# Kernel optimization log

Measured on AMD Instinct MI355X. Metric: run time of the kernel, lower is better.

The kernel has to match this reference:

```python
import jax, jax.numpy as jnp
import numpy as np

N_EMBD = 2048
N_HEAD = 8          # config.n_head // 2
HEAD_DIM = 256      # n_embd // (n_head // 2)
HALF = HEAD_DIM // 2
LAMBDA_INIT = 0.8
RMS_EPS = 1.1920929e-07  # torch float32 finfo eps (F.rms_norm default)


def _rms_norm(x):
    # F.rms_norm with no weight: x / sqrt(mean(x^2) + eps)
    return x * jax.lax.rsqrt(jnp.mean(x * x, axis=-1, keepdims=True) + RMS_EPS)


def setup_inputs() -> dict:
    key = jax.random.key(0)
    ks = jax.random.split(key, 10)
    B, T, C = 2, 2048, N_EMBD
    x = jax.random.normal(ks[0], (B, T, C), dtype=jnp.float32)
    wq = jax.random.normal(ks[1], (C, C), dtype=jnp.float32) * 0.02
    wk = jax.random.normal(ks[2], (C, C), dtype=jnp.float32) * 0.02
    wv = jax.random.normal(ks[3], (C, C), dtype=jnp.float32) * 0.02
    wo = jax.random.normal(ks[4], (C, C), dtype=jnp.float32) * 0.02
    lq1 = jax.random.normal(ks[5], (HEAD_DIM,), dtype=jnp.float32) * 0.1
    lk1 = jax.random.normal(ks[6], (HEAD_DIM,), dtype=jnp.float32) * 0.1
    lq2 = jax.random.normal(ks[7], (HEAD_DIM,), dtype=jnp.float32) * 0.1
    lk2 = jax.random.normal(ks[8], (HEAD_DIM,), dtype=jnp.float32) * 0.1
    return {"x": x, "wq": wq, "wk": wk, "wv": wv, "wo": wo,
            "lq1": lq1, "lk1": lk1, "lq2": lq2, "lk2": lk2}


def _causal_attn(q, k, v, mask):
    # q,k: [B,H,T,half], v: [B,H,T,HEAD_DIM]
    scale = 1.0 / jnp.sqrt(jnp.asarray(q.shape[-1], q.dtype))
    scores = jnp.einsum('bhqd,bhkd->bhqk', q, k) * scale
    scores = jnp.where(mask, scores, -jnp.inf)
    attn = jax.nn.softmax(scores, axis=-1)
    return jnp.einsum('bhqk,bhkd->bhqd', attn, v)


def reference(x, wq, wk, wv, wo, lq1, lk1, lq2, lk2):
    B, T, C = x.shape
    lambda_1 = jnp.exp(jnp.sum(lq1 * lk1))
    lambda_2 = jnp.exp(jnp.sum(lq2 * lk2))
    lambda_full = lambda_1 - lambda_2 + LAMBDA_INIT

    q = (x @ wq.T).reshape(B, T, N_HEAD, 2, HALF).transpose(0, 2, 1, 3, 4)  # [B,H,T,2,half]
    k = (x @ wk.T).reshape(B, T, N_HEAD, 2, HALF).transpose(0, 2, 1, 3, 4)
    v = (x @ wv.T).reshape(B, T, N_HEAD, HEAD_DIM).transpose(0, 2, 1, 3)    # [B,H,T,hd]

    q1 = _rms_norm(q[..., 0, :]); q2 = _rms_norm(q[..., 1, :])
    k1 = _rms_norm(k[..., 0, :]); k2 = _rms_norm(k[..., 1, :])

    mask = jnp.tril(jnp.ones((T, T), dtype=bool))
    y1 = _causal_attn(q1, k1, v, mask)
    y2 = _causal_attn(q2, k2, v, mask)
    y = y1 - lambda_full * y2                                               # [B,H,T,hd]

    y = y.transpose(0, 2, 1, 3).reshape(B, T, C)
    return (y @ wo.T) * (1.0 - LAMBDA_INIT)
```

## Files before the change

kernel.cpp:

```cpp
#include <hip/hip_runtime.h>
#include <stdint.h>


typedef __bf16 bf16;
typedef bf16 bf16x8 __attribute__((ext_vector_type(8)));
typedef bf16 bf16x4 __attribute__((ext_vector_type(4)));
typedef float f32x4 __attribute__((ext_vector_type(4)));

typedef void __attribute__((address_space(1)))* gas_t;
typedef void __attribute__((address_space(3)))* las_t;

__device__ __forceinline__ void gload16(const void* g, void* l) {
  __builtin_amdgcn_global_load_lds((gas_t)(uintptr_t)g, (las_t)(uint32_t)(uintptr_t)l, 16, 0, 0);
}

__device__ __forceinline__ f32x4 mfma16x16(bf16x8 a, bf16x8 b, f32x4 c) {
  return __builtin_amdgcn_mfma_f32_16x16x32_bf16(a, b, c, 0, 0, 0);
}

__global__ __launch_bounds__(256) void cast_all(const float* __restrict__ x,
                                                const float* __restrict__ wq, const float* __restrict__ wk,
                                                const float* __restrict__ wv, const float* __restrict__ wo,
                                                const float* __restrict__ lq1, const float* __restrict__ lk1,
                                                const float* __restrict__ lq2, const float* __restrict__ lk2,
                                                bf16* __restrict__ xb,
                                                bf16* __restrict__ wqb, bf16* __restrict__ wkb,
                                                bf16* __restrict__ wvb, bf16* __restrict__ wob,
                                                float* __restrict__ lam) {
  __shared__ float red[8];
  int tid = threadIdx.x;
  int i = blockIdx.x * 256 + tid;
  const float* in;
  bf16* out;
  int j;
  if (i < 2097152) {
    in = x; out = xb; j = i;
  } else {
    int k = i - 2097152;
    int w = k >> 20;
    j = k & 1048575;
    in = (w == 0) ? wq : (w == 1) ? wk : (w == 2) ? wv : wo;
    out = (w == 0) ? wqb : (w == 1) ? wkb : (w == 2) ? wvb : wob;
  }
  float4 v = ((const float4*)in)[j];
  bf16x4 o;
  o[0] = (bf16)v.x; o[1] = (bf16)v.y; o[2] = (bf16)v.z; o[3] = (bf16)v.w;
  ((bf16x4*)out)[j] = o;

  if (blockIdx.x == 0) {
    float a = lq1[tid] * lk1[tid];
    float b = lq2[tid] * lk2[tid];
#pragma unroll
    for (int m = 32; m >= 1; m >>= 1) {
      a += __shfl_xor(a, m, 64);
      b += __shfl_xor(b, m, 64);
    }
    if ((tid & 63) == 0) { red[tid >> 6] = a; red[4 + (tid >> 6)] = b; }
    __syncthreads();
    if (tid == 0) {
      float s1 = red[0] + red[1] + red[2] + red[3];
      float s2 = red[4] + red[5] + red[6] + red[7];
      lam[0] = expf(s1) - expf(s2) + 0.8f;
    }
  }
}

__global__ __launch_bounds__(512, 2) void gemm_qkv8(const bf16* __restrict__ A,
                                                    const bf16* __restrict__ Bq,
                                                    const bf16* __restrict__ Bk,
                                                    const bf16* __restrict__ Bv,
                                                    bf16* __restrict__ Cq, bf16* __restrict__ Ck,
                                                    bf16* __restrict__ Cv) {
  __shared__ char lds[98304];
  const int K = 2048, nt = 64;

  int p = blockIdx.y * gridDim.x + blockIdx.x;
  int lid = (p & 7) * 48 + (p >> 3);
  const int bm = (lid / 24) * 256;
  const int bnG = (lid % 24) * 256;
  const int z = bnG >> 11;
  const int bn = bnG & 2047;
  const bf16* B = (z == 0) ? Bq : ((z == 1) ? Bk : Bv);

  const int tid = threadIdx.x;
  const int wid = tid >> 6, lane = tid & 63;
  const int l15 = lane & 15, lhi = lane >> 4;
  const int wm = wid >> 2, wn = wid & 3;

  const bf16* aS0 = A + (size_t)(bm + wid * 16 + l15) * K + lhi * 8;
  const bf16* bS0 = B + (size_t)(bn + wid * 16 + l15) * K + lhi * 8;

  auto stA = [&](int t, int pb) {
    char* d = lds + pb * 32768 + wid * 1024;
    const bf16* s = aS0 + t * 32;
    gload16(s, d);
    gload16(s + (size_t)128 * K, d + 8192);
  };
  auto stB = [&](int t, int pb) {
    char* d = lds + pb * 32768 + 16384 + wid * 1024;
    const bf16* s = bS0 + t * 32;
    gload16(s, d);
    gload16(s + (size_t)128 * K, d + 8192);
  };

  const f32x4 fz = {0.f, 0.f, 0.f, 0.f};
  f32x4 acc[8][4];
#pragma unroll
  for (int m = 0; m < 8; ++m)
#pragma unroll
    for (int n = 0; n < 4; ++n) acc[m][n] = fz;

  stA(0, 0); stB(0, 0);
  stA(1, 1); stB(1, 1);
  asm volatile("s_waitcnt vmcnt(4)" ::: "memory");
  __builtin_amdgcn_s_barrier();

  int cur = 0;
  for (int t = 0; t < nt; ++t) {
    const char* ab = lds + cur * 32768;
    const char* bb = ab + 16384;
    int nx2 = cur + 2; if (nx2 >= 3) nx2 -= 3;
    bf16x8 a[8], b0, b1;

#pragma unroll
    for (int m = 0; m < 8; ++m) a[m] = *(const bf16x8*)(ab + (wm * 8 + m) * 1024 + lane * 16);
    b0 = *(const bf16x8*)(bb + (wn * 4 + 0) * 1024 + lane * 16);
    b1 = *(const bf16x8*)(bb + (wn * 4 + 1) * 1024 + lane * 16);
    if (t + 2 < nt) stA(t + 2, nx2);
    __builtin_amdgcn_s_barrier();
    __builtin_amdgcn_s_setprio(1);
#pragma unroll
    for (int m = 0; m < 8; ++m) {
      acc[m][0] = mfma16x16(a[m], b0, acc[m][0]);
      acc[m][1] = mfma16x16(a[m], b1, acc[m][1]);
    }
    __builtin_amdgcn_s_setprio(0);
    __builtin_amdgcn_s_barrier();

    b0 = *(const bf16x8*)(bb + (wn * 4 + 2) * 1024 + lane * 16);
    b1 = *(const bf16x8*)(bb + (wn * 4 + 3) * 1024 + lane * 16);
    if (t + 2 < nt) stB(t + 2, nx2);
    __builtin_amdgcn_s_barrier();
    __builtin_amdgcn_s_setprio(1);
#pragma unroll
    for (int m = 0; m < 8; ++m) {
      acc[m][2] = mfma16x16(a[m], b0, acc[m][2]);
      acc[m][3] = mfma16x16(a[m], b1, acc[m][3]);
    }
    __builtin_amdgcn_s_setprio(0);
    if (t + 2 < nt) {
      asm volatile("s_waitcnt vmcnt(4)" ::: "memory");
    } else {
      asm volatile("s_waitcnt vmcnt(0)" ::: "memory");
    }
    __builtin_amdgcn_s_barrier();

    cur = (cur == 2) ? 0 : cur + 1;
  }

  if (z == 2) {
#pragma unroll
    for (int m = 0; m < 8; ++m)
#pragma unroll
      for (int n = 0; n < 4; ++n)
#pragma unroll
        for (int r = 0; r < 4; ++r) {
          int row = bm + wm * 128 + m * 16 + lhi * 4 + r;
          int col = bn + wn * 64 + n * 16 + l15;
          int bb3 = row >> 11, tt = row & 2047;
          Cv[(size_t)bb3 * 2048 * 2048 + (size_t)col * 2048 + tt] = (bf16)acc[m][n][r];
        }
    return;
  }
  float* ldsf = (float*)lds;
#pragma unroll
  for (int m = 0; m < 8; ++m)
#pragma unroll
    for (int r = 0; r < 4; ++r) {
      float s = acc[m][0][r] * acc[m][0][r] + acc[m][1][r] * acc[m][1][r] +
                acc[m][2][r] * acc[m][2][r] + acc[m][3][r] * acc[m][3][r];
      s += __shfl_xor(s, 1, 64);
      s += __shfl_xor(s, 2, 64);
      s += __shfl_xor(s, 4, 64);
      s += __shfl_xor(s, 8, 64);
      if (l15 == 0) ldsf[(wm * 128 + m * 16 + lhi * 4 + r) * 4 + wn] = s;
    }
  __syncthreads();
  const float osc = (z == 0) ? 0.08838834764831845f : 1.0f;
  bf16* C = (z == 0) ? Cq : Ck;
#pragma unroll
  for (int m = 0; m < 8; ++m) {
#pragma unroll
    for (int r = 0; r < 4; ++r) {
      int rl = wm * 128 + m * 16 + lhi * 4 + r;
      float tot = ldsf[rl * 4 + (wn & 2)] + ldsf[rl * 4 + (wn & 2) + 1];
      float sc = rsqrtf(tot * (1.0f / 128.0f) + 1.1920929e-07f) * osc;
#pragma unroll
      for (int n = 0; n < 4; ++n) {
        int col = bn + wn * 64 + n * 16 + l15;
        C[(size_t)(bm + rl) * 2048 + col] = (bf16)(acc[m][n][r] * sc);
      }
    }
  }
}

__global__ __launch_bounds__(512) void gemm_out(const bf16* __restrict__ A, const bf16* __restrict__ B,
                                                float* __restrict__ Cf) {
  __shared__ char lds[73728];
  const int K = 2048, nt = 64;

  int p = blockIdx.x;
  int lid = (p & 7) * 32 + (p >> 3);
  const int bm = (lid >> 4) * 256;
  const int bn = (lid & 15) * 128;

  const int tid = threadIdx.x;
  const int wid = tid >> 6, lane = tid & 63;
  const int l15 = lane & 15, lhi = lane >> 4;
  const int wm = wid >> 1, wn = wid & 1;

  const bf16* aB = A + (size_t)(bm + wid * 16 + l15) * K + lhi * 8;
  const bf16* bB = B + (size_t)(bn + wid * 16 + l15) * K + lhi * 8;

  auto stage = [&](int t, int pb) {
    char* base = lds + pb * 24576;
    const int k0 = t * 32;
    gload16(aB + k0, base + wid * 1024);
    gload16(aB + (size_t)128 * K + k0, base + 8192 + wid * 1024);
    gload16(bB + k0, base + 16384 + wid * 1024);
  };

  const f32x4 fz = {0.f, 0.f, 0.f, 0.f};
  f32x4 acc[4][4];
#pragma unroll
  for (int m = 0; m < 4; ++m)
#pragma unroll
    for (int n = 0; n < 4; ++n) acc[m][n] = fz;

  stage(0, 0);
  stage(1, 1);
  asm volatile("s_waitcnt vmcnt(3)" ::: "memory");
  __builtin_amdgcn_s_barrier();

  for (int t = 0; t < nt; ++t) {
    const char* ab = lds + (t % 3) * 24576;
    if (t + 2 < nt) stage(t + 2, (t + 2) % 3);
    bf16x8 a[4], b[4];
#pragma unroll
    for (int m = 0; m < 4; ++m)
      a[m] = *(const bf16x8*)(ab + (wm * 4 + m) * 1024 + lane * 16);
#pragma unroll
    for (int n = 0; n < 4; ++n)
      b[n] = *(const bf16x8*)(ab + 16384 + (wn * 4 + n) * 1024 + lane * 16);
    __builtin_amdgcn_s_setprio(1);
#pragma unroll
    for (int m = 0; m < 4; ++m)
#pragma unroll
      for (int n = 0; n < 4; ++n) acc[m][n] = mfma16x16(a[m], b[n], acc[m][n]);
    __builtin_amdgcn_s_setprio(0);
    if (t + 2 < nt) {
      asm volatile("s_waitcnt vmcnt(3)" ::: "memory");
    } else {
      asm volatile("s_waitcnt vmcnt(0)" ::: "memory");
    }
    __builtin_amdgcn_s_barrier();
  }

#pragma unroll
  for (int m = 0; m < 4; ++m)
#pragma unroll
    for (int n = 0; n < 4; ++n)
#pragma unroll
      for (int r = 0; r < 4; ++r) {
        int row = bm + wm * 64 + m * 16 + lhi * 4 + r;
        int col = bn + wn * 64 + n * 16 + l15;
        Cf[(size_t)row * 2048 + col] = acc[m][n][r] * 0.2f;
      }
}

__global__ __launch_bounds__(512, 4) void attn_kernel(const bf16* __restrict__ qb, const bf16* __restrict__ kb,
                                                      const bf16* __restrict__ vtb, bf16* __restrict__ yb,
                                                      const float* __restrict__ lamp) {
  __shared__ char lds[73728];
  const int tid = threadIdx.x;
  const int wid = tid >> 6, lane = tid & 63;
  const int l15 = lane & 15, lhi = lane >> 4;
  char* pl = lds + 65536 + wid * 1024;
  const int s = wid >> 2;
  const int rg = wid & 3;

  const int p = blockIdx.x;
  const int bh = p & 15;
  const int qt = (p < 256) ? (31 - (p >> 4)) : ((p - 256) >> 4);
  const int b = bh >> 3, h = bh & 7;
  const int wr0 = qt * 64 + rg * 16;
  const float lam = lamp[0];

  bf16x8 qf[4];
  {
    const bf16* qrow = qb + (size_t)(b * 2048 + wr0 + l15) * 2048 + h * 256 + s * 128 + lhi * 8;
#pragma unroll
    for (int c = 0; c < 4; ++c) qf[c] = *(const bf16x8*)(qrow + c * 32);
  }

  const f32x4 fz = {0.f, 0.f, 0.f, 0.f};
  f32x4 y[16];
#pragma unroll
  for (int f = 0; f < 16; ++f) y[f] = fz;
  float lsum[4] = {0.f, 0.f, 0.f, 0.f};

  const int nkt = 2 * qt + 2;
  const bf16* kbase = kb + (size_t)(b * 2048) * 2048 + h * 256;
  const bf16* vbase = vtb + (size_t)b * 2048 * 2048 + (size_t)(h * 256) * 2048;

  auto stage = [&](int kt2, int pp) {
    const int t0 = kt2 * 32;
#pragma unroll
    for (int c = 0; c < 2; ++c) {
      int cc = wid * 2 + c;
      int ss = cc >> 3, tg = (cc >> 2) & 1, kc = cc & 3;
      const bf16* sp = kbase + (size_t)(t0 + tg * 16 + l15) * 2048 + ss * 128 + kc * 32 + lhi * 8;
      gload16(sp, lds + pp * 16384 + ss * 8192 + tg * 4096 + kc * 1024);
    }
#pragma unroll
    for (int c = 0; c < 2; ++c) {
      int cc = wid * 2 + c;
      int i = cc >> 2, w4 = cc & 3;
      const bf16* vp = vbase + (size_t)(i * 64 + w4 * 16 + l15) * 2048 + t0 + lhi * 8;
      gload16(vp, lds + 32768 + pp * 16384 + cc * 1024);
    }
  };

  stage(0, 0);
  __syncthreads();

  for (int kt = 0; kt < nkt; ++kt) {
    const int cur = kt & 1;
    const int t0 = kt * 32;
    const bool active = (t0 <= wr0 + 15);
    if (kt + 1 < nkt) stage(kt + 1, cur ^ 1);
    if (active) {
      const char* kc = lds + cur * 16384 + s * 8192;
      const char* vc = lds + 32768 + cur * 16384;
      f32x4 sg[2];
      __builtin_amdgcn_s_setprio(1);
#pragma unroll
      for (int g = 0; g < 2; ++g) {
        f32x4 a = fz;
#pragma unroll
        for (int ks = 0; ks < 4; ++ks)
          a = mfma16x16(qf[ks], *(const bf16x8*)(kc + (g * 4096 + ks * 1024) + lane * 16), a);
        sg[g] = a;
      }
      __builtin_amdgcn_s_setprio(0);
      if (t0 + 31 > wr0) {
#pragma unroll
        for (int g = 0; g < 2; ++g) {
          int col = t0 + g * 16 + l15;
#pragma unroll
          for (int r = 0; r < 4; ++r) {
            int row = wr0 + lhi * 4 + r;
            if (col > row) sg[g][r] = -1e30f;
          }
        }
      }
#pragma unroll
      for (int g = 0; g < 2; ++g)
#pragma unroll
        for (int r = 0; r < 4; ++r) {
          float pv = __expf(sg[g][r] - 12.0f);
          lsum[r] += pv;
          *(bf16*)(pl + ((lhi * 4 + r) * 32 + g * 16 + l15) * 2) = (bf16)pv;
        }
      bf16x8 pa = *(const bf16x8*)(pl + (l15 * 32 + lhi * 8) * 2);
      __builtin_amdgcn_s_setprio(1);
#pragma unroll
      for (int f = 0; f < 16; ++f) {
        bf16x8 vf = *(const bf16x8*)(vc + (f * 64 + lane) * 16);
        y[f] = mfma16x16(pa, vf, y[f]);
      }
      __builtin_amdgcn_s_setprio(0);
    }
    __syncthreads();
  }

  float inv[4];
#pragma unroll
  for (int r = 0; r < 4; ++r) {
    float sv = lsum[r];
    sv += __shfl_xor(sv, 1, 64);
    sv += __shfl_xor(sv, 2, 64);
    sv += __shfl_xor(sv, 4, 64);
    sv += __shfl_xor(sv, 8, 64);
    inv[r] = (s == 0) ? (1.f / sv) : (lam / sv);
  }
  __syncthreads();
  float* yx = (float*)lds;
  if (s == 0) {
#pragma unroll
    for (int f = 0; f < 16; ++f)
#pragma unroll
      for (int r = 0; r < 4; ++r) {
        int rl = rg * 16 + lhi * 4 + r;
        yx[rl * 256 + f * 16 + l15] = y[f][r] * inv[r];
      }
  }
  __syncthreads();
  if (s == 1) {
#pragma unroll
    for (int r = 0; r < 4; ++r) {
      int rl = rg * 16 + lhi * 4 + r;
      bf16* orow = yb + (size_t)(b * 2048 + qt * 64 + rl) * 2048 + h * 256 + l15;
#pragma unroll
      for (int f = 0; f < 16; ++f) {
        float v = yx[rl * 256 + f * 16 + l15] - y[f][r] * inv[r];
        orow[f * 16] = (bf16)v;
      }
    }
  }
}

extern "C" void kernel_launch(void* const* d_in, const int* in_sizes, int n_in,
                              void* d_out, int out_size, void* d_ws, size_t ws_size,
                              hipStream_t stream) {
  const float* x = (const float*)d_in[0];
  const float* wq = (const float*)d_in[1];
  const float* wk = (const float*)d_in[2];
  const float* wv = (const float*)d_in[3];
  const float* wo = (const float*)d_in[4];
  const float* lq1 = (const float*)d_in[5];
  const float* lk1 = (const float*)d_in[6];
  const float* lq2 = (const float*)d_in[7];
  const float* lk2 = (const float*)d_in[8];
  float* out = (float*)d_out;
  char* ws = (char*)d_ws;

  if (ws_size < 117440516) return;

  bf16* xb = (bf16*)(ws + 0);
  bf16* wqb = (bf16*)(ws + 16777216);
  bf16* wkb = (bf16*)(ws + 25165824);
  bf16* wvb = (bf16*)(ws + 33554432);
  bf16* wob = (bf16*)(ws + 41943040);
  bf16* qbuf = (bf16*)(ws + 50331648);
  bf16* kbuf = (bf16*)(ws + 67108864);
  bf16* vtb = (bf16*)(ws + 83886080);
  bf16* ybuf = (bf16*)(ws + 100663296);
  float* lam = (float*)(ws + 117440512);

  cast_all<<<24576, 256, 0, stream>>>(x, wq, wk, wv, wo, lq1, lk1, lq2, lk2,
                                      xb, wqb, wkb, wvb, wob, lam);

  gemm_qkv8<<<dim3(24, 16), 512, 0, stream>>>(xb, wqb, wkb, wvb, qbuf, kbuf, vtb);

  attn_kernel<<<512, 512, 0, stream>>>(qbuf, kbuf, vtb, ybuf, lam);

  gemm_out<<<256, 512, 0, stream>>>(ybuf, wob, out);
}
```

Baseline: 301.5 us.

## Shrink QKV GEMM tile to 256x128 with a simpler single-stage pipeline

Retiles the fused QKV projection GEMM from 256x256 to 256x128 output tiles. This doubles the grid to 768 one-dimensional blocks with an XCD-aware block-to-tile mapping, and raises the launch-bounds occupancy hint. The main loop now stages A and B together and runs one 4x4 MFMA block per k-step with a single barrier, instead of the split half-B schedule with several barriers. The RMS-norm reduction is adjusted to two column-waves per row. The aim is better load balance across CUs and less synchronisation, at the cost of lower operand reuse per tile and more global and LDS traffic.

After: 305.6 us. About the same (+1.4%).

```diff
diff --git a/kernel.cpp b/kernel.cpp
--- a/kernel.cpp
+++ b/kernel.cpp
@@ -65,19 +65,19 @@
   }
 }
 
-__global__ __launch_bounds__(512, 2) void gemm_qkv8(const bf16* __restrict__ A,
+__global__ __launch_bounds__(512, 4) void gemm_qkv3(const bf16* __restrict__ A,
                                                     const bf16* __restrict__ Bq,
                                                     const bf16* __restrict__ Bk,
                                                     const bf16* __restrict__ Bv,
                                                     bf16* __restrict__ Cq, bf16* __restrict__ Ck,
                                                     bf16* __restrict__ Cv) {
-  __shared__ char lds[98304];
+  __shared__ char lds[73728];
   const int K = 2048, nt = 64;
 
-  int p = blockIdx.y * gridDim.x + blockIdx.x;
-  int lid = (p & 7) * 48 + (p >> 3);
-  const int bm = (lid / 24) * 256;
-  const int bnG = (lid % 24) * 256;
+  const int p = blockIdx.x;
+  const int xcd = p & 7, loc = p >> 3;
+  const int bm = (loc / 6) * 256;
+  const int bnG = (xcd * 6 + (loc % 6)) * 128;
   const int z = bnG >> 11;
   const int bn = bnG & 2047;
   const bf16* B = (z == 0) ? Bq : ((z == 1) ? Bk : Bv);
@@ -85,87 +85,63 @@
   const int tid = threadIdx.x;
   const int wid = tid >> 6, lane = tid & 63;
   const int l15 = lane & 15, lhi = lane >> 4;
-  const int wm = wid >> 2, wn = wid & 3;
-
-  const bf16* aS0 = A + (size_t)(bm + wid * 16 + l15) * K + lhi * 8;
-  const bf16* bS0 = B + (size_t)(bn + wid * 16 + l15) * K + lhi * 8;
-
-  auto stA = [&](int t, int pb) {
-    char* d = lds + pb * 32768 + wid * 1024;
-    const bf16* s = aS0 + t * 32;
-    gload16(s, d);
-    gload16(s + (size_t)128 * K, d + 8192);
+  const int wm = wid >> 1, wn = wid & 1;
+
+  const bf16* aB = A + (size_t)(bm + wid * 16 + l15) * K + lhi * 8;
+  const bf16* bB = B + (size_t)(bn + wid * 16 + l15) * K + lhi * 8;
+
+  auto stage = [&](int t, int pb) {
+    char* base = lds + pb * 24576;
+    const int k0 = t * 32;
+    gload16(aB + k0, base + wid * 1024);
+    gload16(aB + (size_t)128 * K + k0, base + 8192 + wid * 1024);
+    gload16(bB + k0, base + 16384 + wid * 1024);
   };
-  auto stB = [&](int t, int pb) {
-    char* d = lds + pb * 32768 + 16384 + wid * 1024;
-    const bf16* s = bS0 + t * 32;
-    gload16(s, d);
-    gload16(s + (size_t)128 * K, d + 8192);
-  };
 
   const f32x4 fz = {0.f, 0.f, 0.f, 0.f};
-  f32x4 acc[8][4];
-#pragma unroll
-  for (int m = 0; m < 8; ++m)
+  f32x4 acc[4][4];
+#pragma unroll
+  for (int m = 0; m < 4; ++m)
 #pragma unroll
     for (int n = 0; n < 4; ++n) acc[m][n] = fz;
 
-  stA(0, 0); stB(0, 0);
-  stA(1, 1); stB(1, 1);
-  asm volatile("s_waitcnt vmcnt(4)" ::: "memory");
+  stage(0, 0);
+  stage(1, 1);
+  asm volatile("s_waitcnt vmcnt(3)" ::: "memory");
   __builtin_amdgcn_s_barrier();
 
-  int cur = 0;
   for (int t = 0; t < nt; ++t) {
-    const char* ab = lds + cur * 32768;
-    const char* bb = ab + 16384;
-    int nx2 = cur + 2; if (nx2 >= 3) nx2 -= 3;
-    bf16x8 a[8], b0, b1;
-
-#pragma unroll
-    for (int m = 0; m < 8; ++m) a[m] = *(const bf16x8*)(ab + (wm * 8 + m) * 1024 + lane * 16);
-    b0 = *(const bf16x8*)(bb + (wn * 4 + 0) * 1024 + lane * 16);
-    b1 = *(const bf16x8*)(bb + (wn * 4 + 1) * 1024 + lane * 16);
-    if (t + 2 < nt) stA(t + 2, nx2);
-    __builtin_amdgcn_s_barrier();
+    const char* ab = lds + (t % 3) * 24576;
+    if (t + 2 < nt) stage(t + 2, (t + 2) % 3);
+    bf16x8 a[4], b[4];
+#pragma unroll
+    for (int m = 0; m < 4; ++m)
+      a[m] = *(const bf16x8*)(ab + (wm * 4 + m) * 1024 + lane * 16);
+#pragma unroll
+    for (int n = 0; n < 4; ++n)
+      b[n] = *(const bf16x8*)(ab + 16384 + (wn * 4 + n) * 1024 + lane * 16);
     __builtin_amdgcn_s_setprio(1);
 #pragma unroll
-    for (int m = 0; m < 8; ++m) {
-      acc[m][0] = mfma16x16(a[m], b0, acc[m][0]);
-      acc[m][1] = mfma16x16(a[m], b1, acc[m][1]);
-    }
-    __builtin_amdgcn_s_setprio(0);
-    __builtin_amdgcn_s_barrier();
-
-    b0 = *(const bf16x8*)(bb + (wn * 4 + 2) * 1024 + lane * 16);
-    b1 = *(const bf16x8*)(bb + (wn * 4 + 3) * 1024 + lane * 16);
-    if (t + 2 < nt) stB(t + 2, nx2);
-    __builtin_amdgcn_s_barrier();
-    __builtin_amdgcn_s_setprio(1);
-#pragma unroll
-    for (int m = 0; m < 8; ++m) {
-      acc[m][2] = mfma16x16(a[m], b0, acc[m][2]);
-      acc[m][3] = mfma16x16(a[m], b1, acc[m][3]);
-    }
+    for (int m = 0; m < 4; ++m)
+#pragma unroll
+      for (int n = 0; n < 4; ++n) acc[m][n] = mfma16x16(a[m], b[n], acc[m][n]);
     __builtin_amdgcn_s_setprio(0);
     if (t + 2 < nt) {
-      asm volatile("s_waitcnt vmcnt(4)" ::: "memory");
+      asm volatile("s_waitcnt vmcnt(3)" ::: "memory");
     } else {
       asm volatile("s_waitcnt vmcnt(0)" ::: "memory");
     }
     __builtin_amdgcn_s_barrier();
-
-    cur = (cur == 2) ? 0 : cur + 1;
   }
 
   if (z == 2) {
 #pragma unroll
-    for (int m = 0; m < 8; ++m)
+    for (int m = 0; m < 4; ++m)
 #pragma unroll
       for (int n = 0; n < 4; ++n)
 #pragma unroll
         for (int r = 0; r < 4; ++r) {
-          int row = bm + wm * 128 + m * 16 + lhi * 4 + r;
+          int row = bm + wm * 64 + m * 16 + lhi * 4 + r;
           int col = bn + wn * 64 + n * 16 + l15;
           int bb3 = row >> 11, tt = row & 2047;
           Cv[(size_t)bb3 * 2048 * 2048 + (size_t)col * 2048 + tt] = (bf16)acc[m][n][r];
@@ -174,26 +150,27 @@
   }
   float* ldsf = (float*)lds;
 #pragma unroll
-  for (int m = 0; m < 8; ++m)
+  for (int m = 0; m < 4; ++m)
 #pragma unroll
     for (int r = 0; r < 4; ++r) {
-      float s = acc[m][0][r] * acc[m][0][r] + acc[m][1][r] * acc[m][1][r] +
-                acc[m][2][r] * acc[m][2][r] + acc[m][3][r] * acc[m][3][r];
+      float s = 0.f;
+#pragma unroll
+      for (int n = 0; n < 4; ++n) s += acc[m][n][r] * acc[m][n][r];
       s += __shfl_xor(s, 1, 64);
       s += __shfl_xor(s, 2, 64);
       s += __shfl_xor(s, 4, 64);
       s += __shfl_xor(s, 8, 64);
-      if (l15 == 0) ldsf[(wm * 128 + m * 16 + lhi * 4 + r) * 4 + wn] = s;
+      if (l15 == 0) ldsf[(wm * 64 + m * 16 + lhi * 4 + r) * 2 + wn] = s;
     }
   __syncthreads();
   const float osc = (z == 0) ? 0.08838834764831845f : 1.0f;
   bf16* C = (z == 0) ? Cq : Ck;
 #pragma unroll
-  for (int m = 0; m < 8; ++m) {
+  for (int m = 0; m < 4; ++m)
 #pragma unroll
     for (int r = 0; r < 4; ++r) {
-      int rl = wm * 128 + m * 16 + lhi * 4 + r;
-      float tot = ldsf[rl * 4 + (wn & 2)] + ldsf[rl * 4 + (wn & 2) + 1];
+      int rl = wm * 64 + m * 16 + lhi * 4 + r;
+      float tot = ldsf[rl * 2] + ldsf[rl * 2 + 1];
       float sc = rsqrtf(tot * (1.0f / 128.0f) + 1.1920929e-07f) * osc;
 #pragma unroll
       for (int n = 0; n < 4; ++n) {
@@ -201,7 +178,6 @@
         C[(size_t)(bm + rl) * 2048 + col] = (bf16)(acc[m][n][r] * sc);
       }
     }
-  }
 }
 
 __global__ __launch_bounds__(512) void gemm_out(const bf16* __restrict__ A, const bf16* __restrict__ B,
@@ -451,7 +427,7 @@
   cast_all<<<24576, 256, 0, stream>>>(x, wq, wk, wv, wo, lq1, lk1, lq2, lk2,
                                       xb, wqb, wkb, wvb, wob, lam);
 
-  gemm_qkv8<<<dim3(24, 16), 512, 0, stream>>>(xb, wqb, wkb, wvb, qbuf, kbuf, vtb);
+  gemm_qkv3<<<768, 512, 0, stream>>>(xb, wqb, wkb, wvb, qbuf, kbuf, vtb);
 
   attn_kernel<<<512, 512, 0, stream>>>(qbuf, kbuf, vtb, ybuf, lam);
 
```
